# Performance work log

Measured on AMD Instinct MI355X. Metric: run time of the kernel, lower is better.

The kernel has to match this reference:

```python
import jax, jax.numpy as jnp
import numpy as np

D = 256      # feature_dim (d_model)
H = 4        # num_heads
N = 4096     # query nodes
M = 4096     # source nodes


def _conv1x1(W, b, x):
    # Conv1d(kernel_size=1): per-position linear over channels. x: [1, Cin, N]
    return jnp.einsum('oi,bin->bon', W, x) + b[None, :, None]


def setup_inputs() -> dict:
    key = jax.random.key(0)
    ks = jax.random.split(key, 16)
    s = 0.02
    inp = {
        'x':      jax.random.normal(ks[0], (1, D, N), jnp.float32),
        'source': jax.random.normal(ks[1], (1, D, M), jnp.float32),
        'dist':   jax.random.uniform(ks[2], (1, N, M), jnp.float32),
        'mask':   jax.random.bernoulli(ks[3], 0.5, (N, M)),
        'Wq': s * jax.random.normal(ks[4], (D, D), jnp.float32),  'bq': jnp.zeros((D,), jnp.float32),
        'Wk': s * jax.random.normal(ks[5], (D, D), jnp.float32),  'bk': jnp.zeros((D,), jnp.float32),
        'Wv': s * jax.random.normal(ks[6], (D, D), jnp.float32),  'bv': jnp.zeros((D,), jnp.float32),
        'Wm': s * jax.random.normal(ks[7], (D, D), jnp.float32),  'bm': jnp.zeros((D,), jnp.float32),
        'W1': s * jax.random.normal(ks[8], (2 * D, 2 * D), jnp.float32), 'b1': jnp.zeros((2 * D,), jnp.float32),
        'W2': s * jax.random.normal(ks[9], (D, 2 * D), jnp.float32),     'b2': jnp.zeros((D,), jnp.float32),
    }
    return inp


def reference(x, source, dist, mask, Wq, bq, Wk, bk, Wv, bv, Wm, bm, W1, b1, W2, b2):
    dim = D // H  # per-head dim; torch view(1, dim, H, -1) splits channels as (dim, H)
    q = _conv1x1(Wq, bq, x).reshape(1, dim, H, N)
    k = _conv1x1(Wk, bk, source).reshape(1, dim, H, M)
    v = _conv1x1(Wv, bv, source).reshape(1, dim, H, M)

    scores = jnp.einsum('bdhn,bdhm->bhnm', q, k) / jnp.sqrt(jnp.asarray(dim, q.dtype))
    # non-standard additive mask: global detached min scales the masked-out entries
    smin = jax.lax.stop_gradient(scores.min())
    scores = scores + smin * (~mask).astype(scores.dtype)[None, None, :, :]

    prob = jax.nn.softmax(scores, axis=-1)                       # [1,H,N,M]
    attn = jnp.einsum('bhnm,bdhm->bdhn', prob, v)                # [1,dim,H,N]
    message = _conv1x1(Wm, bm, attn.reshape(1, D, N))            # merge heads

    h = jnp.concatenate([x, message], axis=1)                    # [1,2D,N]
    h = jax.nn.relu(_conv1x1(W1, b1, h))
    y = _conv1x1(W2, b2, h)                                      # [1,D,N]
    weights = scores.mean(axis=1)                                # [1,N,M]
    return y, weights
```

## Files before the change

### kernel.cpp

```cpp
#include <hip/hip_runtime.h>
#include <hip/hip_bf16.h>
#include <math.h>

#define Dm 256
#define Hh 4
#define Nn 4096
#define Mq 4096

typedef __attribute__((ext_vector_type(8))) short bf16x8;
typedef __attribute__((ext_vector_type(4))) float f32x4;

#define MFMA_BF16(a,b,c) __builtin_amdgcn_mfma_f32_16x16x32_bf16(a,b,c,0,0,0)

#define MB (1u<<20)
#define OFF_FLAG  0
#define OFF_SMIN  64
#define OFF_PART  1024
#define OFF_MT    (64u<<10)
#define OFF_DENP  (128u<<10)
#define OFF_STATS (512u<<10)
#define OFF_WB    (1u*MB)
#define OFF_BITS  (5u*MB/2)
#define OFF_QB    (9u*MB/2)
#define OFF_KB    (13u*MB/2)
#define OFF_VB    (17u*MB/2)
#define OFF_HCAT  (21u*MB/2)
#define OFF_ATTNT (29u*MB/2)
#define OFF_XT    (33u*MB/2)
#define OFF_ST    (37u*MB/2)
#define OFF_OPART (33u*MB/2)
#define OFF_H1T   (33u*MB/2)

#define WOFF_Q  0
#define WOFF_K  65536
#define WOFF_V  131072
#define WOFF_M  196608
#define WOFF_1  262144
#define WOFF_2  524288

__device__ __forceinline__ unsigned short f2bf(float x) {
    unsigned u = __float_as_uint(x);
    u += 0x7FFF + ((u >> 16) & 1);
    return (unsigned short)(u >> 16);
}
__device__ __forceinline__ float bf2f(unsigned short b) {
    return __uint_as_float(((unsigned)b) << 16);
}

__global__ void k_detect(const unsigned char* __restrict__ mb, int* __restrict__ flag) {
    __shared__ int c[5];
    if (threadIdx.x < 5) c[threadIdx.x] = 0;
    __syncthreads();
    for (int i = threadIdx.x; i < 16384; i += blockDim.x) {
        unsigned char b = mb[i];
        if (b) {
            atomicAdd(&c[i & 3], 1);
            if ((i & 7) == 4) atomicAdd(&c[4], 1);
        }
    }
    __syncthreads();
    if (threadIdx.x == 0) {
        int f;
        if (c[3] > 0 && c[0] == 0)          f = 3;
        else if (c[1] | c[2] | c[3])        f = 1;
        else if (c[4] > 0)                  f = 0;
        else                                f = 2;
        *flag = f;
    }
}

__global__ void k_maskbits(const void* __restrict__ mp, const int* __restrict__ flagp,
                           unsigned char* __restrict__ bits) {
    size_t i = (size_t)blockIdx.x * 256 + threadIdx.x;
    const int flag = *flagp;
    size_t base = i * 8;
    unsigned b = 0;
    if (flag == 1) {
        unsigned long long u = *(const unsigned long long*)((const unsigned char*)mp + base);
        #pragma unroll
        for (int j = 0; j < 8; j++) b |= (unsigned)(((u >> (8*j)) & 0xFFull) != 0ull) << j;
    } else if (flag == 0) {
        const int* p = (const int*)mp;
        #pragma unroll
        for (int j = 0; j < 8; j++) b |= (unsigned)(p[base + j] != 0) << j;
    } else if (flag == 3) {
        const float* p = (const float*)mp;
        #pragma unroll
        for (int j = 0; j < 8; j++) b |= (unsigned)(p[base + j] != 0.0f) << j;
    } else {
        const unsigned long long* p = (const unsigned long long*)mp;
        #pragma unroll
        for (int j = 0; j < 8; j++) b |= (unsigned)(p[base + j] != 0ull) << j;
    }
    bits[i] = (unsigned char)b;
}

__global__ __launch_bounds__(256) void k_prep(const float* __restrict__ src,
                                              unsigned short* __restrict__ dst,
                                              unsigned short* __restrict__ dst2) {
    const int l = threadIdx.x & 63, g = threadIdx.x >> 6;
    const int c = blockIdx.y * 64 + l;
    const int n0 = blockIdx.x * 32 + g * 8;
    float4 v0 = *(const float4*)(src + (size_t)c * Nn + n0);
    float4 v1 = *(const float4*)(src + (size_t)c * Nn + n0 + 4);
    float vv[8] = {v0.x, v0.y, v0.z, v0.w, v1.x, v1.y, v1.z, v1.w};
    #pragma unroll
    for (int j = 0; j < 8; j++) {
        unsigned short b = f2bf(vv[j]);
        dst[(size_t)(n0 + j) * 256 + c] = b;
        if (dst2) dst2[(size_t)(n0 + j) * 512 + c] = b;
    }
}

__global__ void k_wcast(const float* __restrict__ Wq, const float* __restrict__ Wk,
                        const float* __restrict__ Wv, const float* __restrict__ Wm,
                        const float* __restrict__ W1, const float* __restrict__ W2,
                        unsigned short* __restrict__ wb) {
    size_t i = (size_t)blockIdx.x * 256 + threadIdx.x;
    const float* s; size_t off;
    if      (i < 131072 && i < 65536) { s = Wq; off = i; }
    else if (i < 131072)              { s = Wk; off = i - 65536; }
    else if (i < 196608)              { s = Wv; off = i - 131072; }
    else if (i < 262144)              { s = Wm; off = i - 196608; }
    else if (i < 524288)              { s = W1; off = i - 262144; }
    else                              { s = W2; off = i - 524288; }
    wb[i] = f2bf(s[off]);
}

template<int KK, int MODE>
__global__ __launch_bounds__(256) void k_mgemm(const unsigned short* __restrict__ wb,
                                               const float* __restrict__ bias,
                                               const unsigned short* __restrict__ xt,
                                               void* __restrict__ out) {
    const int tid = threadIdx.x, w = tid >> 6, lane = tid & 63;
    const int lg = lane >> 4, lr = lane & 15;
    const int o_base = blockIdx.y * 64 + w * 16;
    const int n_base = blockIdx.x * 64;
    f32x4 acc[4];
    #pragma unroll
    for (int j = 0; j < 4; j++) acc[j] = (f32x4){0.f, 0.f, 0.f, 0.f};
    const unsigned short* wrow = wb + (size_t)(o_base + lr) * KK + lg * 8;
    const unsigned short* xrow = xt + (size_t)(n_base + lr) * KK + lg * 8;
    #pragma unroll
    for (int k0 = 0; k0 < KK; k0 += 32) {
        bf16x8 af = *(const bf16x8*)(wrow + k0);
        #pragma unroll
        for (int j = 0; j < 4; j++) {
            bf16x8 bfr = *(const bf16x8*)(xrow + (size_t)j * 16 * KK + k0);
            acc[j] = MFMA_BF16(af, bfr, acc[j]);
        }
    }
    float bv[4];
    #pragma unroll
    for (int r = 0; r < 4; r++) bv[r] = bias[o_base + lg * 4 + r];
    #pragma unroll
    for (int j = 0; j < 4; j++) {
        #pragma unroll
        for (int r = 0; r < 4; r++) {
            int o = o_base + lg * 4 + r;
            int n = n_base + j * 16 + lr;
            float v = acc[j][r] + bv[r];
            if (MODE == 0) {
                ((float*)out)[(size_t)o * Nn + n] = v;
            } else if (MODE == 1) {
                ((unsigned short*)out)[(((size_t)(o & 3)) * Nn + n) * 64 + (o >> 2)] = f2bf(v);
            } else if (MODE == 2) {
                ((unsigned short*)out)[(((size_t)(o & 3)) * 64 + (o >> 2)) * Nn + n] = f2bf(v);
            } else if (MODE == 3) {
                ((unsigned short*)out)[(size_t)n * 512 + 256 + o] = f2bf(v);
            } else {
                ((unsigned short*)out)[(size_t)n * 512 + o] = f2bf(fmaxf(v, 0.f));
            }
        }
    }
}

__global__ __launch_bounds__(256) void k_pass1(
    const unsigned short* __restrict__ qb, const unsigned short* __restrict__ kb,
    const unsigned long long* __restrict__ bits,
    float* __restrict__ stats, float* __restrict__ partial) {
    const int tid = threadIdx.x;
    const int wv = tid >> 6, lane = tid & 63;
    const int h = wv;
    const int lg = lane >> 4, lr = lane & 15;
    const int n0 = blockIdx.x * 32;
    const int m0 = blockIdx.y * 1024;

    bf16x8 qf[2][2];
    #pragma unroll
    for (int ns = 0; ns < 2; ns++)
        #pragma unroll
        for (int ks = 0; ks < 2; ks++)
            qf[ns][ks] = *(const bf16x8*)(qb + (((size_t)h * Nn + n0 + ns*16 + lr) << 6) + ks*32 + lg*8);

    const unsigned long long* brow0 = bits + (((size_t)(n0 + lr)) << 6) + (m0 >> 6);
    const unsigned long long* brow1 = bits + (((size_t)(n0 + 16 + lr)) << 6) + (m0 >> 6);

    float mn = INFINITY;
    float mx1[2] = {-INFINITY, -INFINITY};
    float mx0[2] = {-INFINITY, -INFINITY};
    unsigned long long bw[2] = {0ull, 0ull};

    for (int ms = 0; ms < 64; ms++) {
        const size_t krow = ((size_t)h * Mq + m0 + ms*16 + lr) << 6;
        bf16x8 a0 = *(const bf16x8*)(kb + krow + lg*8);
        bf16x8 a1 = *(const bf16x8*)(kb + krow + 32 + lg*8);
        if ((ms & 3) == 0) { bw[0] = brow0[ms >> 2]; bw[1] = brow1[ms >> 2]; }
        const int shbase = (ms & 3) * 16 + lg * 4;
        #pragma unroll
        for (int ns = 0; ns < 2; ns++) {
            f32x4 acc = {0.f, 0.f, 0.f, 0.f};
            acc = MFMA_BF16(a0, qf[ns][0], acc);
            acc = MFMA_BF16(a1, qf[ns][1], acc);
            #pragma unroll
            for (int r = 0; r < 4; r++) {
                float v = acc[r] * 0.125f;
                mn = fminf(mn, v);
                bool b = (bw[ns] >> (shbase + r)) & 1ull;
                mx1[ns] = fmaxf(mx1[ns], b ? v : -INFINITY);
                mx0[ns] = fmaxf(mx0[ns], b ? -INFINITY : v);
            }
        }
    }
    #pragma unroll
    for (int ns = 0; ns < 2; ns++) {
        mx1[ns] = fmaxf(mx1[ns], __shfl_xor(mx1[ns], 16));
        mx1[ns] = fmaxf(mx1[ns], __shfl_xor(mx1[ns], 32));
        mx0[ns] = fmaxf(mx0[ns], __shfl_xor(mx0[ns], 16));
        mx0[ns] = fmaxf(mx0[ns], __shfl_xor(mx0[ns], 32));
    }
    if (lane < 16) {
        #pragma unroll
        for (int ns = 0; ns < 2; ns++) {
            size_t row = (size_t)h * Nn + n0 + ns*16 + lane;
            stats[(row*4 + blockIdx.y)*2 + 0] = mx1[ns];
            stats[(row*4 + blockIdx.y)*2 + 1] = mx0[ns];
        }
    }
    for (int off = 1; off < 64; off <<= 1) mn = fminf(mn, __shfl_xor(mn, off));
    __shared__ float wmin[4];
    if (lane == 0) wmin[wv] = mn;
    __syncthreads();
    if (tid == 0)
        partial[blockIdx.x*4 + blockIdx.y] = fminf(fminf(wmin[0], wmin[1]), fminf(wmin[2], wmin[3]));
}

__global__ void k_minreduce(const float* __restrict__ partial, float* __restrict__ smin) {
    const int tid = threadIdx.x;
    float mn = fminf(partial[tid], partial[tid + 256]);
    __shared__ float red[256];
    red[tid] = mn;
    __syncthreads();
    for (int st = 128; st > 0; st >>= 1) {
        if (tid < st) red[tid] = fminf(red[tid], red[tid + st]);
        __syncthreads();
    }
    if (tid == 0) *smin = red[0];
}

__global__ void k_rowfix(const float* __restrict__ stats, const float* __restrict__ sminp,
                         float* __restrict__ mtarr) {
    int row = blockIdx.x * 256 + threadIdx.x;
    float smin = *sminp;
    float mt = -INFINITY;
    #pragma unroll
    for (int mb = 0; mb < 4; mb++) {
        float a = stats[((size_t)row*4 + mb)*2];
        float b = stats[((size_t)row*4 + mb)*2 + 1];
        mt = fmaxf(mt, fmaxf(a, b + smin));
    }
    mtarr[row] = mt;
}

__global__ __launch_bounds__(256) void k_pass2(
    const unsigned short* __restrict__ qb, const unsigned short* __restrict__ kb,
    const unsigned short* __restrict__ vb,
    const unsigned long long* __restrict__ bits,
    const float* __restrict__ sminp, const float* __restrict__ mtarr,
    float* __restrict__ wout, float* __restrict__ denp, unsigned short* __restrict__ opart) {
    __shared__ float swout[4][32][36];
    const int tid = threadIdx.x;
    const int wv = tid >> 6, lane = tid & 63;
    const int h = wv;
    const int lg = lane >> 4, lr = lane & 15;
    const int n0 = blockIdx.x * 32;
    const int m0 = blockIdx.y * 1024;
    const float smin = *sminp;

    bf16x8 qf[2][2];
    #pragma unroll
    for (int ns = 0; ns < 2; ns++)
        #pragma unroll
        for (int ks = 0; ks < 2; ks++)
            qf[ns][ks] = *(const bf16x8*)(qb + (((size_t)h * Nn + n0 + ns*16 + lr) << 6) + ks*32 + lg*8);

    float mt[2];
    mt[0] = mtarr[(size_t)h * Nn + n0 + lr];
    mt[1] = mtarr[(size_t)h * Nn + n0 + 16 + lr];

    const unsigned long long* brow0 = bits + (((size_t)(n0 + lr)) << 6) + (m0 >> 6);
    const unsigned long long* brow1 = bits + (((size_t)(n0 + 16 + lr)) << 6) + (m0 >> 6);

    f32x4 oacc[2][4];
    #pragma unroll
    for (int ns = 0; ns < 2; ns++)
        #pragma unroll
        for (int ds = 0; ds < 4; ds++)
            oacc[ns][ds] = (f32x4){0.f, 0.f, 0.f, 0.f};
    float dsum[2] = {0.f, 0.f};
    unsigned long long bw[2] = {0ull, 0ull};

    for (int cc = 0; cc < 32; cc++) {
        const int mch = m0 + cc * 32;
        if ((cc & 1) == 0) { bw[0] = brow0[cc >> 1]; bw[1] = brow1[cc >> 1]; }
        const int wsh = (cc & 1) * 32;
        #pragma unroll
        for (int msub = 0; msub < 2; msub++) {
            const size_t krow = ((size_t)h * Mq + mch + msub*16 + lr) << 6;
            bf16x8 a0 = *(const bf16x8*)(kb + krow + lg*8);
            bf16x8 a1 = *(const bf16x8*)(kb + krow + 32 + lg*8);
            const int shb = wsh + msub*16 + lg*4;
            #pragma unroll
            for (int ns = 0; ns < 2; ns++) {
                f32x4 acc = {0.f, 0.f, 0.f, 0.f};
                acc = MFMA_BF16(a0, qf[ns][0], acc);
                acc = MFMA_BF16(a1, qf[ns][1], acc);
                f32x4 msk;
                #pragma unroll
                for (int r = 0; r < 4; r++) {
                    bool b = (bw[ns] >> (shb + r)) & 1ull;
                    msk[r] = acc[r] * 0.125f + (b ? 0.f : smin);
                }
                *(f32x4*)&swout[h][ns*16 + lr][msub*16 + lg*4] = msk;
            }
        }
        __syncthreads();
        #pragma unroll
        for (int r4 = 0; r4 < 4; r4++) {
            int idx = r4*256 + tid;
            int nl = idx >> 5, ml = idx & 31;
            float s = swout[0][nl][ml] + swout[1][nl][ml] + swout[2][nl][ml] + swout[3][nl][ml];
            wout[(size_t)(n0 + nl) * Mq + mch + ml] = 0.25f * s;
        }
        bf16x8 vf[4];
        #pragma unroll
        for (int ds = 0; ds < 4; ds++)
            vf[ds] = *(const bf16x8*)(vb + ((size_t)(h*64 + ds*16 + lr)) * Mq + mch + lg*8);
        #pragma unroll
        for (int ns = 0; ns < 2; ns++) {
            const float* srow = &swout[h][ns*16 + lr][lg*8];
            bf16x8 pf;
            #pragma unroll
            for (int i = 0; i < 8; i++) {
                float p = __expf(srow[i] - mt[ns]);
                dsum[ns] += p;
                pf[i] = (short)f2bf(p);
            }
            #pragma unroll
            for (int ds = 0; ds < 4; ds++)
                oacc[ns][ds] = MFMA_BF16(pf, vf[ds], oacc[ns][ds]);
        }
        __syncthreads();
    }
    #pragma unroll
    for (int ns = 0; ns < 2; ns++) {
        dsum[ns] += __shfl_xor(dsum[ns], 16);
        dsum[ns] += __shfl_xor(dsum[ns], 32);
    }
    if (lane < 16) {
        #pragma unroll
        for (int ns = 0; ns < 2; ns++)
            denp[((size_t)h * Nn + n0 + ns*16 + lane)*4 + blockIdx.y] = dsum[ns];
    }
    unsigned short* op = opart + (size_t)blockIdx.y * (Dm * Nn);
    #pragma unroll
    for (int ns = 0; ns < 2; ns++)
        #pragma unroll
        for (int ds = 0; ds < 4; ds++)
            #pragma unroll
            for (int r = 0; r < 4; r++) {
                int dd = ds*16 + lr;
                int n = n0 + ns*16 + lg*4 + r;
                op[(size_t)(dd*4 + h) * Nn + n] = f2bf(oacc[ns][ds][r]);
            }
}

__global__ __launch_bounds__(256) void k_finish(const unsigned short* __restrict__ opart,
                                                const float* __restrict__ denp,
                                                unsigned short* __restrict__ attnT) {
    __shared__ float t[64][65];
    const int cb = blockIdx.y * 64, nb = blockIdx.x * 64;
    const int tid = threadIdx.x;
    #pragma unroll
    for (int e = 0; e < 16; e++) {
        int idx = e * 256 + tid;
        int c_l = idx >> 6, n_l = idx & 63;
        int c = cb + c_l, n = nb + n_l;
        float s = 0.f;
        #pragma unroll
        for (int y = 0; y < 4; y++)
            s += bf2f(opart[(size_t)y * (Dm*Nn) + (size_t)c * Nn + n]);
        size_t row = (size_t)(c & 3) * Nn + n;
        float d = denp[row*4] + denp[row*4+1] + denp[row*4+2] + denp[row*4+3];
        t[c_l][n_l] = s / d;
    }
    __syncthreads();
    #pragma unroll
    for (int e = 0; e < 16; e++) {
        int idx = e * 256 + tid;
        int n_l = idx >> 6, c_l = idx & 63;
        attnT[(size_t)(nb + n_l) * 256 + cb + c_l] = f2bf(t[c_l][n_l]);
    }
}

extern "C" void kernel_launch(void* const* d_in, const int* in_sizes, int n_in,
                              void* d_out, int out_size, void* d_ws, size_t ws_size,
                              hipStream_t stream) {
    const float* x      = (const float*)d_in[0];
    const float* source = (const float*)d_in[1];
    const void*  mask   = d_in[3];
    const float* Wq = (const float*)d_in[4];  const float* bq = (const float*)d_in[5];
    const float* Wk = (const float*)d_in[6];  const float* bk = (const float*)d_in[7];
    const float* Wv = (const float*)d_in[8];  const float* bv = (const float*)d_in[9];
    const float* Wm = (const float*)d_in[10]; const float* bm = (const float*)d_in[11];
    const float* W1 = (const float*)d_in[12]; const float* b1 = (const float*)d_in[13];
    const float* W2 = (const float*)d_in[14]; const float* b2 = (const float*)d_in[15];

    float* y    = (float*)d_out;
    float* wout = y + (size_t)Dm * Nn;

    char* ws = (char*)d_ws;
    int*   flag  = (int*)(ws + OFF_FLAG);
    float* sminp = (float*)(ws + OFF_SMIN);
    float* part  = (float*)(ws + OFF_PART);
    float* mtarr = (float*)(ws + OFF_MT);
    float* denp  = (float*)(ws + OFF_DENP);
    float* stats = (float*)(ws + OFF_STATS);
    unsigned short* wb    = (unsigned short*)(ws + OFF_WB);
    unsigned char*  bits  = (unsigned char*)(ws + OFF_BITS);
    unsigned short* qb    = (unsigned short*)(ws + OFF_QB);
    unsigned short* kb    = (unsigned short*)(ws + OFF_KB);
    unsigned short* vb    = (unsigned short*)(ws + OFF_VB);
    unsigned short* hcat  = (unsigned short*)(ws + OFF_HCAT);
    unsigned short* attnT = (unsigned short*)(ws + OFF_ATTNT);
    unsigned short* xt    = (unsigned short*)(ws + OFF_XT);
    unsigned short* st    = (unsigned short*)(ws + OFF_ST);
    unsigned short* opart = (unsigned short*)(ws + OFF_OPART);
    unsigned short* h1t   = (unsigned short*)(ws + OFF_H1T);

    k_detect<<<1, 256, 0, stream>>>((const unsigned char*)mask, flag);
    k_maskbits<<<8192, 256, 0, stream>>>(mask, flag, bits);

    k_prep<<<dim3(128, 4), 256, 0, stream>>>(x, xt, hcat);
    k_prep<<<dim3(128, 4), 256, 0, stream>>>(source, st, nullptr);
    k_wcast<<<2560, 256, 0, stream>>>(Wq, Wk, Wv, Wm, W1, W2, wb);

    k_mgemm<256, 1><<<dim3(64, 4), 256, 0, stream>>>(wb + WOFF_Q, bq, xt, qb);
    k_mgemm<256, 1><<<dim3(64, 4), 256, 0, stream>>>(wb + WOFF_K, bk, st, kb);
    k_mgemm<256, 2><<<dim3(64, 4), 256, 0, stream>>>(wb + WOFF_V, bv, st, vb);

    k_pass1<<<dim3(128, 4), 256, 0, stream>>>(qb, kb, (const unsigned long long*)bits, stats, part);
    k_minreduce<<<1, 256, 0, stream>>>(part, sminp);
    k_rowfix<<<64, 256, 0, stream>>>(stats, sminp, mtarr);

    k_pass2<<<dim3(128, 4), 256, 0, stream>>>(qb, kb, vb, (const unsigned long long*)bits,
                                              sminp, mtarr, wout, denp, opart);
    k_finish<<<dim3(64, 4), 256, 0, stream>>>(opart, denp, attnT);

    k_mgemm<256, 3><<<dim3(64, 4), 256, 0, stream>>>(wb + WOFF_M, bm, attnT, hcat);
    k_mgemm<512, 4><<<dim3(64, 8), 256, 0, stream>>>(wb + WOFF_1, b1, hcat, h1t);
    k_mgemm<512, 0><<<dim3(64, 4), 256, 0, stream>>>(wb + WOFF_2, b2, h1t, y);
}
```

Baseline: 238.5 us.

## Restructure attention into score, weights and PV kernels with LDS-staged K

Splits the fused second pass into a separate weights-writing score kernel and a PV kernel. Both stage swizzled K tiles in double-buffered shared memory and process all heads, or larger query tiles, per block. The Q/K/V projections are fused into one launch, V is stored in fp16 for f16 MFMA, and the output partials are written as packed 64-bit stores. The intent is better K reuse and less global traffic and fewer syncs, at the cost of recomputing QK^T in an extra pass and a reworked workspace layout.

```diff
diff --git a/kernel.cpp b/kernel.cpp
--- a/kernel.cpp
+++ b/kernel.cpp
@@ -9,27 +9,29 @@
 
 typedef __attribute__((ext_vector_type(8))) short bf16x8;
 typedef __attribute__((ext_vector_type(4))) float f32x4;
+typedef _Float16 __attribute__((ext_vector_type(4))) f16x4;
 
 #define MFMA_BF16(a,b,c) __builtin_amdgcn_mfma_f32_16x16x32_bf16(a,b,c,0,0,0)
+#define MFMA_F16x16(a,b,c) __builtin_amdgcn_mfma_f32_16x16x16f16(a,b,c,0,0,0)
 
 #define MB (1u<<20)
 #define OFF_FLAG  0
 #define OFF_SMIN  64
-#define OFF_PART  1024
-#define OFF_MT    (64u<<10)
+#define OFF_PART  128
+#define OFF_MT    4096
 #define OFF_DENP  (128u<<10)
 #define OFF_STATS (512u<<10)
-#define OFF_WB    (1u*MB)
-#define OFF_BITS  (5u*MB/2)
-#define OFF_QB    (9u*MB/2)
-#define OFF_KB    (13u*MB/2)
-#define OFF_VB    (17u*MB/2)
-#define OFF_HCAT  (21u*MB/2)
-#define OFF_ATTNT (29u*MB/2)
-#define OFF_XT    (33u*MB/2)
-#define OFF_ST    (37u*MB/2)
-#define OFF_OPART (33u*MB/2)
-#define OFF_H1T   (33u*MB/2)
+#define OFF_WB    (3u*MB/2)
+#define OFF_BITS  (3u*MB)
+#define OFF_QB    (5u*MB)
+#define OFF_KB    (7u*MB)
+#define OFF_VB    (9u*MB)
+#define OFF_HCAT  (11u*MB)
+#define OFF_ATTNT (15u*MB)
+#define OFF_XT    (17u*MB)
+#define OFF_ST    (19u*MB)
+#define OFF_OPART (17u*MB)
+#define OFF_H1T   (17u*MB)
 
 #define WOFF_Q  0
 #define WOFF_K  65536
@@ -118,7 +120,7 @@
                         unsigned short* __restrict__ wb) {
     size_t i = (size_t)blockIdx.x * 256 + threadIdx.x;
     const float* s; size_t off;
-    if      (i < 131072 && i < 65536) { s = Wq; off = i; }
+    if      (i < 65536)               { s = Wq; off = i; }
     else if (i < 131072)              { s = Wk; off = i - 65536; }
     else if (i < 196608)              { s = Wv; off = i - 131072; }
     else if (i < 262144)              { s = Wm; off = i - 196608; }
@@ -127,15 +129,16 @@
     wb[i] = f2bf(s[off]);
 }
 
-template<int KK, int MODE>
-__global__ __launch_bounds__(256) void k_mgemm(const unsigned short* __restrict__ wb,
-                                               const float* __restrict__ bias,
-                                               const unsigned short* __restrict__ xt,
-                                               void* __restrict__ out) {
+template<int KK>
+__device__ __forceinline__ void gemm_body(const unsigned short* __restrict__ wb,
+                                          const float* __restrict__ bias,
+                                          const unsigned short* __restrict__ xt,
+                                          void* __restrict__ out, int mode,
+                                          int bx, int by) {
     const int tid = threadIdx.x, w = tid >> 6, lane = tid & 63;
     const int lg = lane >> 4, lr = lane & 15;
-    const int o_base = blockIdx.y * 64 + w * 16;
-    const int n_base = blockIdx.x * 64;
+    const int o_base = by * 64 + w * 16;
+    const int n_base = bx * 64;
     f32x4 acc[4];
     #pragma unroll
     for (int j = 0; j < 4; j++) acc[j] = (f32x4){0.f, 0.f, 0.f, 0.f};
@@ -160,94 +163,179 @@
             int o = o_base + lg * 4 + r;
             int n = n_base + j * 16 + lr;
             float v = acc[j][r] + bv[r];
-            if (MODE == 0) {
+            if (mode == 0) {
                 ((float*)out)[(size_t)o * Nn + n] = v;
-            } else if (MODE == 1) {
+            } else if (mode == 1) {
                 ((unsigned short*)out)[(((size_t)(o & 3)) * Nn + n) * 64 + (o >> 2)] = f2bf(v);
-            } else if (MODE == 2) {
-                ((unsigned short*)out)[(((size_t)(o & 3)) * 64 + (o >> 2)) * Nn + n] = f2bf(v);
-            } else if (MODE == 3) {
+            } else if (mode == 2) {
+                union { _Float16 h; unsigned short u; } cv; cv.h = (_Float16)v;
+                ((unsigned short*)out)[(((size_t)(o & 3)) * 64 + (o >> 2)) * Mq + n] = cv.u;
+            } else if (mode == 3) {
                 ((unsigned short*)out)[(size_t)n * 512 + 256 + o] = f2bf(v);
+            } else if (mode == 4) {
+                ((unsigned short*)out)[(size_t)n * 512 + o] = f2bf(fmaxf(v, 0.f));
             } else {
-                ((unsigned short*)out)[(size_t)n * 512 + o] = f2bf(fmaxf(v, 0.f));
+                int dd = o >> 2, hh = o & 3, g = dd >> 3, pos = dd & 7;
+                int slot = g ^ (n & 7);
+                ((unsigned short*)out)[(((size_t)hh * Mq + n)) * 64 + slot * 8 + pos] = f2bf(v);
             }
         }
     }
 }
 
-__global__ __launch_bounds__(256) void k_pass1(
+template<int KK>
+__global__ __launch_bounds__(256) void k_mgemm(const unsigned short* __restrict__ wb,
+                                               const float* __restrict__ bias,
+                                               const unsigned short* __restrict__ xt,
+                                               void* __restrict__ out, int mode) {
+    gemm_body<KK>(wb, bias, xt, out, mode, blockIdx.x, blockIdx.y);
+}
+
+__global__ __launch_bounds__(256) void k_qkv(const unsigned short* __restrict__ wb,
+                                             const float* __restrict__ bq,
+                                             const float* __restrict__ bk,
+                                             const float* __restrict__ bv,
+                                             const unsigned short* __restrict__ xt,
+                                             const unsigned short* __restrict__ st,
+                                             void* __restrict__ qb, void* __restrict__ kb,
+                                             void* __restrict__ vb) {
+    const int z = blockIdx.z;
+    const float* bias = (z == 0) ? bq : ((z == 1) ? bk : bv);
+    const unsigned short* X = (z == 0) ? xt : st;
+    void* out = (z == 0) ? qb : ((z == 1) ? kb : vb);
+    int mode = (z == 0) ? 1 : ((z == 1) ? 5 : 2);
+    gemm_body<256>(wb + z * 65536, bias, X, out, mode, blockIdx.x, blockIdx.y);
+}
+
+template<int PHASE>
+__global__ __launch_bounds__(512) void k_score(
     const unsigned short* __restrict__ qb, const unsigned short* __restrict__ kb,
     const unsigned long long* __restrict__ bits,
-    float* __restrict__ stats, float* __restrict__ partial) {
+    const float* __restrict__ sminp,
+    float* __restrict__ stats, float* __restrict__ partial,
+    float* __restrict__ wout) {
+    __shared__ unsigned short kbuf[2][8192];
     const int tid = threadIdx.x;
-    const int wv = tid >> 6, lane = tid & 63;
-    const int h = wv;
+    const int w = tid >> 6, lane = tid & 63;
     const int lg = lane >> 4, lr = lane & 15;
-    const int n0 = blockIdx.x * 32;
-    const int m0 = blockIdx.y * 1024;
-
-    bf16x8 qf[2][2];
-    #pragma unroll
-    for (int ns = 0; ns < 2; ns++)
-        #pragma unroll
-        for (int ks = 0; ks < 2; ks++)
-            qf[ns][ks] = *(const bf16x8*)(qb + (((size_t)h * Nn + n0 + ns*16 + lr) << 6) + ks*32 + lg*8);
-
-    const unsigned long long* brow0 = bits + (((size_t)(n0 + lr)) << 6) + (m0 >> 6);
-    const unsigned long long* brow1 = bits + (((size_t)(n0 + 16 + lr)) << 6) + (m0 >> 6);
+    const int n0 = blockIdx.x * 128 + w * 16;
+    const int mb = blockIdx.y;
+    const int m0 = mb * 512;
+
+    bf16x8 qf[4][2];
+    #pragma unroll
+    for (int h = 0; h < 4; h++)
+        #pragma unroll
+        for (int kh = 0; kh < 2; kh++)
+            qf[h][kh] = *(const bf16x8*)(qb + (((size_t)h * Nn + n0 + lr) << 6) + kh*32 + lg*8);
+
+    float smin = 0.f;
+    if (PHASE) smin = *sminp;
+
+    const int h0 = tid >> 8, q0 = tid & 255;
+    const unsigned short* src0 = kb + (((size_t)h0 * Mq + m0) << 6) + q0 * 8;
+    const unsigned short* src1 = kb + (((size_t)(h0 + 2) * Mq + m0) << 6) + q0 * 8;
+    unsigned short* dst0 = &kbuf[0][h0 * 2048 + q0 * 8];
+    unsigned short* dst1 = &kbuf[0][(h0 + 2) * 2048 + q0 * 8];
 
     float mn = INFINITY;
-    float mx1[2] = {-INFINITY, -INFINITY};
-    float mx0[2] = {-INFINITY, -INFINITY};
-    unsigned long long bw[2] = {0ull, 0ull};
-
-    for (int ms = 0; ms < 64; ms++) {
-        const size_t krow = ((size_t)h * Mq + m0 + ms*16 + lr) << 6;
-        bf16x8 a0 = *(const bf16x8*)(kb + krow + lg*8);
-        bf16x8 a1 = *(const bf16x8*)(kb + krow + 32 + lg*8);
-        if ((ms & 3) == 0) { bw[0] = brow0[ms >> 2]; bw[1] = brow1[ms >> 2]; }
-        const int shbase = (ms & 3) * 16 + lg * 4;
-        #pragma unroll
-        for (int ns = 0; ns < 2; ns++) {
-            f32x4 acc = {0.f, 0.f, 0.f, 0.f};
-            acc = MFMA_BF16(a0, qf[ns][0], acc);
-            acc = MFMA_BF16(a1, qf[ns][1], acc);
+    float mx1[4], mx0[4];
+    #pragma unroll
+    for (int h = 0; h < 4; h++) { mx1[h] = -INFINITY; mx0[h] = -INFINITY; }
+
+    const unsigned long long* brow = bits + (((size_t)(n0 + lr)) << 6) + (m0 >> 6);
+    unsigned long long bw = 0ull;
+
+    bf16x8 r0 = *(const bf16x8*)(src0);
+    bf16x8 r1 = *(const bf16x8*)(src1);
+    *(bf16x8*)dst0 = r0;
+    *(bf16x8*)dst1 = r1;
+    __syncthreads();
+    r0 = *(const bf16x8*)(src0 + 2048);
+    r1 = *(const bf16x8*)(src1 + 2048);
+
+    for (int t = 0; t < 16; t++) {
+        const unsigned short* kB = &kbuf[t & 1][0];
+        const int mch = m0 + t * 32;
+        if ((t & 1) == 0) bw = brow[t >> 1];
+        #pragma unroll
+        for (int mi = 0; mi < 2; mi++) {
+            const int rowoff = (mi * 16 + lr) * 64;
+            const int shb = (t & 1) * 32 + mi * 16 + lg * 4;
+            f32x4 ssum = (f32x4){0.f, 0.f, 0.f, 0.f};
             #pragma unroll
-            for (int r = 0; r < 4; r++) {
-                float v = acc[r] * 0.125f;
-                mn = fminf(mn, v);
-                bool b = (bw[ns] >> (shbase + r)) & 1ull;
-                mx1[ns] = fmaxf(mx1[ns], b ? v : -INFINITY);
-                mx0[ns] = fmaxf(mx0[ns], b ? -INFINITY : v);
+            for (int h = 0; h < 4; h++) {
+                bf16x8 a0 = *(const bf16x8*)(kB + h*2048 + rowoff + ((lg ^ (lr & 7)) << 3));
+                bf16x8 a1 = *(const bf16x8*)(kB + h*2048 + rowoff + (((lg + 4) ^ (lr & 7)) << 3));
+                f32x4 acc = (f32x4){0.f, 0.f, 0.f, 0.f};
+                acc = MFMA_BF16(a0, qf[h][0], acc);
+                acc = MFMA_BF16(a1, qf[h][1], acc);
+                if (PHASE == 0) {
+                    #pragma unroll
+                    for (int r = 0; r < 4; r++) {
+                        float v = acc[r] * 0.125f;
+                        mn = fminf(mn, v);
+                        bool b = (bw >> (shb + r)) & 1ull;
+                        mx1[h] = fmaxf(mx1[h], b ? v : -INFINITY);
+                        mx0[h] = fmaxf(mx0[h], b ? -INFINITY : v);
+                    }
+                } else {
+                    ssum += acc;
+                }
             }
-        }
-    }
-    #pragma unroll
-    for (int ns = 0; ns < 2; ns++) {
-        mx1[ns] = fmaxf(mx1[ns], __shfl_xor(mx1[ns], 16));
-        mx1[ns] = fmaxf(mx1[ns], __shfl_xor(mx1[ns], 32));
-        mx0[ns] = fmaxf(mx0[ns], __shfl_xor(mx0[ns], 16));
-        mx0[ns] = fmaxf(mx0[ns], __shfl_xor(mx0[ns], 32));
-    }
-    if (lane < 16) {
-        #pragma unroll
-        for (int ns = 0; ns < 2; ns++) {
-            size_t row = (size_t)h * Nn + n0 + ns*16 + lane;
-            stats[(row*4 + blockIdx.y)*2 + 0] = mx1[ns];
-            stats[(row*4 + blockIdx.y)*2 + 1] = mx0[ns];
-        }
-    }
-    for (int off = 1; off < 64; off <<= 1) mn = fminf(mn, __shfl_xor(mn, off));
-    __shared__ float wmin[4];
-    if (lane == 0) wmin[wv] = mn;
-    __syncthreads();
-    if (tid == 0)
-        partial[blockIdx.x*4 + blockIdx.y] = fminf(fminf(wmin[0], wmin[1]), fminf(wmin[2], wmin[3]));
+            if (PHASE == 1) {
+                f32x4 wv;
+                #pragma unroll
+                for (int r = 0; r < 4; r++) {
+                    bool b = (bw >> (shb + r)) & 1ull;
+                    wv[r] = ssum[r] * 0.03125f + (b ? 0.f : smin);
+                }
+                *(f32x4*)(wout + (size_t)(n0 + lr) * Mq + mch + mi * 16 + lg * 4) = wv;
+            }
+        }
+        if (t < 15) {
+            *(bf16x8*)(dst0 + (((t + 1) & 1) ? 8192 : 0)) = r0;
+            *(bf16x8*)(dst1 + (((t + 1) & 1) ? 8192 : 0)) = r1;
+        }
+        __syncthreads();
+        if (t < 14) {
+            r0 = *(const bf16x8*)(src0 + (size_t)(t + 2) * 2048);
+            r1 = *(const bf16x8*)(src1 + (size_t)(t + 2) * 2048);
+        }
+    }
+
+    if (PHASE == 0) {
+        #pragma unroll
+        for (int h = 0; h < 4; h++) {
+            mx1[h] = fmaxf(mx1[h], __shfl_xor(mx1[h], 16));
+            mx1[h] = fmaxf(mx1[h], __shfl_xor(mx1[h], 32));
+            mx0[h] = fmaxf(mx0[h], __shfl_xor(mx0[h], 16));
+            mx0[h] = fmaxf(mx0[h], __shfl_xor(mx0[h], 32));
+        }
+        if (lane < 16) {
+            #pragma unroll
+            for (int h = 0; h < 4; h++) {
+                size_t row = (size_t)h * Nn + n0 + lane;
+                stats[row * 16 + mb * 2 + 0] = mx1[h];
+                stats[row * 16 + mb * 2 + 1] = mx0[h];
+            }
+        }
+        for (int off = 1; off < 64; off <<= 1) mn = fminf(mn, __shfl_xor(mn, off));
+        __shared__ float wmin[8];
+        if (lane == 0) wmin[w] = mn;
+        __syncthreads();
+        if (tid == 0) {
+            float m2 = wmin[0];
+            #pragma unroll
+            for (int i = 1; i < 8; i++) m2 = fminf(m2, wmin[i]);
+            partial[blockIdx.x * 8 + mb] = m2;
+        }
+    }
 }
 
 __global__ void k_minreduce(const float* __restrict__ partial, float* __restrict__ smin) {
     const int tid = threadIdx.x;
-    float mn = fminf(partial[tid], partial[tid + 256]);
+    float mn = partial[tid];
     __shared__ float red[256];
     red[tid] = mn;
     __syncthreads();
@@ -264,125 +352,121 @@
     float smin = *sminp;
     float mt = -INFINITY;
     #pragma unroll
-    for (int mb = 0; mb < 4; mb++) {
-        float a = stats[((size_t)row*4 + mb)*2];
-        float b = stats[((size_t)row*4 + mb)*2 + 1];
+    for (int mb = 0; mb < 8; mb++) {
+        float a = stats[(size_t)row * 16 + mb * 2];
+        float b = stats[(size_t)row * 16 + mb * 2 + 1];
         mt = fmaxf(mt, fmaxf(a, b + smin));
     }
     mtarr[row] = mt;
 }
 
-__global__ __launch_bounds__(256) void k_pass2(
+__global__ __launch_bounds__(512) void k_pv(
     const unsigned short* __restrict__ qb, const unsigned short* __restrict__ kb,
-    const unsigned short* __restrict__ vb,
+    const unsigned short* __restrict__ vbh,
     const unsigned long long* __restrict__ bits,
     const float* __restrict__ sminp, const float* __restrict__ mtarr,
-    float* __restrict__ wout, float* __restrict__ denp, unsigned short* __restrict__ opart) {
-    __shared__ float swout[4][32][36];
+    float* __restrict__ denp, unsigned short* __restrict__ opart) {
+    __shared__ unsigned short kbuf[2][4096];
     const int tid = threadIdx.x;
-    const int wv = tid >> 6, lane = tid & 63;
-    const int h = wv;
+    const int w = tid >> 6, lane = tid & 63;
     const int lg = lane >> 4, lr = lane & 15;
-    const int n0 = blockIdx.x * 32;
-    const int m0 = blockIdx.y * 1024;
+    const int h = blockIdx.y & 3, mb = (blockIdx.y >> 2) & 3, dh = blockIdx.y >> 4;
+    const int n0 = blockIdx.x * 512 + w * 64;
+    const int m0 = mb * 1024;
     const float smin = *sminp;
 
-    bf16x8 qf[2][2];
-    #pragma unroll
-    for (int ns = 0; ns < 2; ns++)
-        #pragma unroll
-        for (int ks = 0; ks < 2; ks++)
-            qf[ns][ks] = *(const bf16x8*)(qb + (((size_t)h * Nn + n0 + ns*16 + lr) << 6) + ks*32 + lg*8);
-
-    float mt[2];
-    mt[0] = mtarr[(size_t)h * Nn + n0 + lr];
-    mt[1] = mtarr[(size_t)h * Nn + n0 + 16 + lr];
-
-    const unsigned long long* brow0 = bits + (((size_t)(n0 + lr)) << 6) + (m0 >> 6);
-    const unsigned long long* brow1 = bits + (((size_t)(n0 + 16 + lr)) << 6) + (m0 >> 6);
-
-    f32x4 oacc[2][4];
-    #pragma unroll
-    for (int ns = 0; ns < 2; ns++)
-        #pragma unroll
-        for (int ds = 0; ds < 4; ds++)
-            oacc[ns][ds] = (f32x4){0.f, 0.f, 0.f, 0.f};
-    float dsum[2] = {0.f, 0.f};
-    unsigned long long bw[2] = {0ull, 0ull};
-
-    for (int cc = 0; cc < 32; cc++) {
-        const int mch = m0 + cc * 32;
-        if ((cc & 1) == 0) { bw[0] = brow0[cc >> 1]; bw[1] = brow1[cc >> 1]; }
-        const int wsh = (cc & 1) * 32;
-        #pragma unroll
-        for (int msub = 0; msub < 2; msub++) {
-            const size_t krow = ((size_t)h * Mq + mch + msub*16 + lr) << 6;
-            bf16x8 a0 = *(const bf16x8*)(kb + krow + lg*8);
-            bf16x8 a1 = *(const bf16x8*)(kb + krow + 32 + lg*8);
-            const int shb = wsh + msub*16 + lg*4;
+    bf16x8 qf[4][2];
+    float mt[4];
+    #pragma unroll
+    for (int ns = 0; ns < 4; ns++) {
+        #pragma unroll
+        for (int kh = 0; kh < 2; kh++)
+            qf[ns][kh] = *(const bf16x8*)(qb + (((size_t)h * Nn + n0 + ns*16 + lr) << 6) + kh*32 + lg*8);
+        mt[ns] = mtarr[(size_t)h * Nn + n0 + ns*16 + lr];
+    }
+
+    f32x4 oacc[4][2];
+    float dsum[4];
+    #pragma unroll
+    for (int ns = 0; ns < 4; ns++) {
+        oacc[ns][0] = (f32x4){0.f,0.f,0.f,0.f};
+        oacc[ns][1] = (f32x4){0.f,0.f,0.f,0.f};
+        dsum[ns] = 0.f;
+    }
+
+    const unsigned short* ksrc = kb + (((size_t)h * Mq + m0) << 6) + tid * 8;
+    bf16x8 r0 = *(const bf16x8*)(ksrc);
+    *(bf16x8*)&kbuf[0][tid * 8] = r0;
+    __syncthreads();
+    r0 = *(const bf16x8*)(ksrc + 4096);
+
+    const unsigned short* vrow0 = vbh + ((size_t)(h * 64 + dh * 32 + lr)) * Mq;
+    const unsigned short* vrow1 = vbh + ((size_t)(h * 64 + dh * 32 + 16 + lr)) * Mq;
+
+    for (int t = 0; t < 16; t++) {
+        const unsigned short* kB = &kbuf[t & 1][0];
+        const int mch = m0 + t * 64;
+        unsigned long long bw[4];
+        #pragma unroll
+        for (int ns = 0; ns < 4; ns++)
+            bw[ns] = bits[(((size_t)(n0 + ns*16 + lr)) << 6) + (mch >> 6)];
+        #pragma unroll
+        for (int mi = 0; mi < 4; mi++) {
+            const int rowoff = (mi * 16 + lr) * 64;
+            bf16x8 a0 = *(const bf16x8*)(kB + rowoff + ((lg ^ (lr & 7)) << 3));
+            bf16x8 a1 = *(const bf16x8*)(kB + rowoff + (((lg + 4) ^ (lr & 7)) << 3));
+            f16x4 vf0 = *(const f16x4*)(vrow0 + mch + mi * 16 + lg * 4);
+            f16x4 vf1 = *(const f16x4*)(vrow1 + mch + mi * 16 + lg * 4);
+            const int shb = mi * 16 + lg * 4;
             #pragma unroll
-            for (int ns = 0; ns < 2; ns++) {
-                f32x4 acc = {0.f, 0.f, 0.f, 0.f};
+            for (int ns = 0; ns < 4; ns++) {
+                f32x4 acc = (f32x4){0.f,0.f,0.f,0.f};
                 acc = MFMA_BF16(a0, qf[ns][0], acc);
                 acc = MFMA_BF16(a1, qf[ns][1], acc);
-                f32x4 msk;
+                f16x4 pf;
+                float dloc = 0.f;
                 #pragma unroll
                 for (int r = 0; r < 4; r++) {
                     bool b = (bw[ns] >> (shb + r)) & 1ull;
-                    msk[r] = acc[r] * 0.125f + (b ? 0.f : smin);
+                    float v = acc[r] * 0.125f + (b ? 0.f : smin);
+                    float p = __expf(v - mt[ns]);
+                    dloc += p;
+                    pf[r] = (_Float16)p;
                 }
-                *(f32x4*)&swout[h][ns*16 + lr][msub*16 + lg*4] = msk;
+                dsum[ns] += dloc;
+                oacc[ns][0] = MFMA_F16x16(pf, vf0, oacc[ns][0]);
+                oacc[ns][1] = MFMA_F16x16(pf, vf1, oacc[ns][1]);
             }
         }
+        if (t < 15) *(bf16x8*)&kbuf[(t + 1) & 1][tid * 8] = r0;
         __syncthreads();
-        #pragma unroll
-        for (int r4 = 0; r4 < 4; r4++) {
-            int idx = r4*256 + tid;
-            int nl = idx >> 5, ml = idx & 31;
-            float s = swout[0][nl][ml] + swout[1][nl][ml] + swout[2][nl][ml] + swout[3][nl][ml];
-            wout[(size_t)(n0 + nl) * Mq + mch + ml] = 0.25f * s;
-        }
-        bf16x8 vf[4];
-        #pragma unroll
-        for (int ds = 0; ds < 4; ds++)
-            vf[ds] = *(const bf16x8*)(vb + ((size_t)(h*64 + ds*16 + lr)) * Mq + mch + lg*8);
-        #pragma unroll
-        for (int ns = 0; ns < 2; ns++) {
-            const float* srow = &swout[h][ns*16 + lr][lg*8];
-            bf16x8 pf;
-            #pragma unroll
-            for (int i = 0; i < 8; i++) {
-                float p = __expf(srow[i] - mt[ns]);
-                dsum[ns] += p;
-                pf[i] = (short)f2bf(p);
-            }
-            #pragma unroll
-            for (int ds = 0; ds < 4; ds++)
-                oacc[ns][ds] = MFMA_BF16(pf, vf[ds], oacc[ns][ds]);
-        }
-        __syncthreads();
-    }
-    #pragma unroll
-    for (int ns = 0; ns < 2; ns++) {
+        if (t < 14) r0 = *(const bf16x8*)(ksrc + (size_t)(t + 2) * 4096);
+    }
+
+    #pragma unroll
+    for (int ns = 0; ns < 4; ns++) {
         dsum[ns] += __shfl_xor(dsum[ns], 16);
         dsum[ns] += __shfl_xor(dsum[ns], 32);
     }
-    if (lane < 16) {
-        #pragma unroll
-        for (int ns = 0; ns < 2; ns++)
-            denp[((size_t)h * Nn + n0 + ns*16 + lane)*4 + blockIdx.y] = dsum[ns];
-    }
-    unsigned short* op = opart + (size_t)blockIdx.y * (Dm * Nn);
-    #pragma unroll
-    for (int ns = 0; ns < 2; ns++)
-        #pragma unroll
-        for (int ds = 0; ds < 4; ds++)
-            #pragma unroll
-            for (int r = 0; r < 4; r++) {
-                int dd = ds*16 + lr;
-                int n = n0 + ns*16 + lg*4 + r;
-                op[(size_t)(dd*4 + h) * Nn + n] = f2bf(oacc[ns][ds][r]);
-            }
+    if (dh == 0 && lane < 16) {
+        #pragma unroll
+        for (int ns = 0; ns < 4; ns++)
+            denp[((size_t)h * Nn + n0 + ns*16 + lane) * 4 + mb] = dsum[ns];
+    }
+    unsigned short* op = opart + (size_t)mb * (Dm * Nn);
+    #pragma unroll
+    for (int ns = 0; ns < 4; ns++)
+        #pragma unroll
+        for (int ds = 0; ds < 2; ds++) {
+            int c = (dh * 32 + ds * 16 + lr) * 4 + h;
+            int n = n0 + ns * 16 + lg * 4;
+            unsigned long long pk =
+                (unsigned long long)f2bf(oacc[ns][ds][0]) |
+                ((unsigned long long)f2bf(oacc[ns][ds][1]) << 16) |
+                ((unsigned long long)f2bf(oacc[ns][ds][2]) << 32) |
+                ((unsigned long long)f2bf(oacc[ns][ds][3]) << 48);
+            *(unsigned long long*)&op[(size_t)c * Nn + n] = pk;
+        }
 }
 
 __global__ __launch_bounds__(256) void k_finish(const unsigned short* __restrict__ opart,
@@ -455,19 +539,21 @@
     k_prep<<<dim3(128, 4), 256, 0, stream>>>(source, st, nullptr);
     k_wcast<<<2560, 256, 0, stream>>>(Wq, Wk, Wv, Wm, W1, W2, wb);
 
-    k_mgemm<256, 1><<<dim3(64, 4), 256, 0, stream>>>(wb + WOFF_Q, bq, xt, qb);
-    k_mgemm<256, 1><<<dim3(64, 4), 256, 0, stream>>>(wb + WOFF_K, bk, st, kb);
-    k_mgemm<256, 2><<<dim3(64, 4), 256, 0, stream>>>(wb + WOFF_V, bv, st, vb);
-
-    k_pass1<<<dim3(128, 4), 256, 0, stream>>>(qb, kb, (const unsigned long long*)bits, stats, part);
+    k_qkv<<<dim3(64, 4, 3), 256, 0, stream>>>(wb, bq, bk, bv, xt, st, qb, kb, vb);
+
+    k_score<0><<<dim3(32, 8), 512, 0, stream>>>(qb, kb, (const unsigned long long*)bits,
+                                                nullptr, stats, part, nullptr);
     k_minreduce<<<1, 256, 0, stream>>>(part, sminp);
     k_rowfix<<<64, 256, 0, stream>>>(stats, sminp, mtarr);
 
-    k_pass2<<<dim3(128, 4), 256, 0, stream>>>(qb, kb, vb, (const unsigned long long*)bits,
-                                              sminp, mtarr, wout, denp, opart);
+    k_score<1><<<dim3(32, 8), 512, 0, stream>>>(qb, kb, (const unsigned long long*)bits,
+                                                sminp, nullptr, nullptr, wout);
+
+    k_pv<<<dim3(8, 32), 512, 0, stream>>>(qb, kb, vb, (const unsigned long long*)bits,
+                                          sminp, mtarr, denp, opart);
     k_finish<<<dim3(64, 4), 256, 0, stream>>>(opart, denp, attnT);
 
-    k_mgemm<256, 3><<<dim3(64, 4), 256, 0, stream>>>(wb + WOFF_M, bm, attnT, hcat);
-    k_mgemm<512, 4><<<dim3(64, 8), 256, 0, stream>>>(wb + WOFF_1, b1, hcat, h1t);
-    k_mgemm<512, 0><<<dim3(64, 4), 256, 0, stream>>>(wb + WOFF_2, b2, h1t, y);
-}
+    k_mgemm<256><<<dim3(64, 4), 256, 0, stream>>>(wb + WOFF_M, bm, attnT, hcat, 3);
+    k_mgemm<512><<<dim3(64, 8), 256, 0, stream>>>(wb + WOFF_1, b1, hcat, h1t, 4);
+    k_mgemm<512><<<dim3(64, 4), 256, 0, stream>>>(wb + WOFF_2, b2, h1t, y, 0);
+}
```

Measured after the change: 235.3 us. About the same (-1.3%).
